# Kernel tuning notes

Measured on AMD Instinct MI355X. Metric: run time of the kernel, lower is better.

The kernel has to match this reference:

```python
import jax, jax.numpy as jnp
import numpy as np

TEMPERATURE = 0.07
EPS = 1e-8  # torch cosine_similarity clamps the norm product at eps


def setup_inputs() -> dict:
    key = jax.random.key(0)
    k1, k2 = jax.random.split(key)
    B, D = 8192, 256
    u = jax.random.normal(k1, (B, D), dtype=jnp.float32)
    v = jax.random.normal(k2, (B, D), dtype=jnp.float32)
    return {"u": u, "v": v}


def _cos_sim_matrix(a, b):
    # pairwise cosine similarity: (a . b) / max(|a||b|, eps)
    dots = a @ b.T                                   # [B, B]
    an = jnp.linalg.norm(a, axis=-1)                 # [B]
    bn = jnp.linalg.norm(b, axis=-1)                 # [B]
    denom = jnp.maximum(an[:, None] * bn[None, :], EPS)
    return dots / denom


def reference(u, v):
    B = u.shape[0]
    sim_uv = _cos_sim_matrix(u, v) / TEMPERATURE     # [B, B]
    sim_uu = _cos_sim_matrix(u, u) / TEMPERATURE     # [B, B]
    eye = jnp.eye(B, dtype=bool)
    pos_loss = jnp.diagonal(sim_uv)                  # [B]
    neg_inf = jnp.array(-jnp.inf, dtype=sim_uv.dtype)
    # off-diagonal entries of both matrices, concatenated per row (2B-2 valid each)
    negative_sim = jnp.concatenate(
        [jnp.where(eye, neg_inf, sim_uv), jnp.where(eye, neg_inf, sim_uu)], axis=1
    )                                                # [B, 2B]
    neg_loss = jax.nn.logsumexp(negative_sim, axis=-1)  # [B]
    return (-pos_loss + neg_loss).mean()
```

## Files before the change

kernel.cpp:

```cpp
#include <hip/hip_runtime.h>
#include <hip/hip_bf16.h>
#include <stdint.h>

#define NB 8192
#define ND 256
#define NW 16384
#define BM 128
#define BN 128
#define NSTRIP 4
#define STRIPW 4096
#define NTILES (STRIPW / BN)
#define NBLK 256
#define SQRT_L2E_INVT 4.5398164f
#define LN2F 0.69314718056f

typedef float floatx4 __attribute__((ext_vector_type(4)));
typedef int   intx4   __attribute__((ext_vector_type(4)));
typedef int   intx8   __attribute__((ext_vector_type(8)));

__device__ __forceinline__ void gload_lds16(const void* g, void* l) {
    __builtin_amdgcn_global_load_lds(
        (const __attribute__((address_space(1))) unsigned int*)g,
        (__attribute__((address_space(3))) unsigned int*)l,
        16, 0, 0);
}

__global__ __launch_bounds__(512) void prep_kernel(
    const float* __restrict__ u, const float* __restrict__ v,
    unsigned char* __restrict__ W, int* __restrict__ cnt)
{
    if (blockIdx.x == 0 && threadIdx.x == 0) *cnt = 0;
    const int t    = threadIdx.x;
    const int row  = blockIdx.x * 8 + (t >> 6);
    const int lane = t & 63;
    const float* src = (row < NB) ? (v + (size_t)row * ND)
                                  : (u + (size_t)(row - NB) * ND);
    float4 x = ((const float4*)src)[lane];
    float ss = x.x * x.x + x.y * x.y + x.z * x.z + x.w * x.w;
#pragma unroll
    for (int off = 1; off < 64; off <<= 1) ss += __shfl_xor(ss, off, 64);
    const float sc = rsqrtf(ss) * SQRT_L2E_INVT;
    int p = __builtin_amdgcn_cvt_pk_fp8_f32(x.x * sc, x.y * sc, 0, false);
    p     = __builtin_amdgcn_cvt_pk_fp8_f32(x.z * sc, x.w * sc, p, true);
    ((int*)(W + (size_t)row * ND))[lane] = p;
}

__global__ __launch_bounds__(512, 2) void dcl_main(
    const unsigned char* __restrict__ W,
    float* __restrict__ partial,
    float* __restrict__ pos,
    int* __restrict__ cnt,
    float* __restrict__ out)
{
    const int b  = blockIdx.x;
    const int s  = (b >> 1) & 3;
    const int rt = ((b >> 3) << 1) | (b & 1);
    const int rb = rt * BM;

    const unsigned char* A = W + (size_t)NB * ND;

    __shared__ __align__(16) char lds[98304];

    const int tid  = threadIdx.x;
    const int wave = tid >> 6;
    const int lane = tid & 63;
    const int wm   = wave >> 2;
    const int wn   = wave & 3;
    const int quad = lane >> 4;
    const int tcol = lane & 15;

    {
        const int cb0 = s * STRIPW;
#pragma unroll
        for (int i = 0; i < 4; i++) {
            int o = i * 8192 + wave * 1024 + lane * 16;
            int r = o >> 8;
            int c = (o >> 4) & 15;
            int cg = (c ^ (r & 15)) * 16;
            gload_lds16(A + (size_t)(rb + r) * ND + cg,
                        lds + i * 8192 + wave * 1024);
            gload_lds16(W + (size_t)(cb0 + r) * ND + cg,
                        lds + 32768 + i * 8192 + wave * 1024);
        }
    }
    __syncthreads();

    intx8 af[4][2];
#pragma unroll
    for (int mt = 0; mt < 4; mt++) {
        int r = wm * 64 + mt * 16 + tcol;
#pragma unroll
        for (int ks = 0; ks < 2; ks++) {
            int c0 = ks * 8 + quad * 2;
            intx4 lo = *(const intx4*)(lds + r * 256 + ((c0 ^ (r & 15)) << 4));
            intx4 hi = *(const intx4*)(lds + r * 256 + (((c0 + 1) ^ (r & 15)) << 4));
            intx8 f;
            f[0] = lo[0]; f[1] = lo[1]; f[2] = lo[2]; f[3] = lo[3];
            f[4] = hi[0]; f[5] = hi[1]; f[6] = hi[2]; f[7] = hi[3];
            af[mt][ks] = f;
        }
    }

    float rsum[4][4];
#pragma unroll
    for (int mt = 0; mt < 4; mt++)
#pragma unroll
        for (int reg = 0; reg < 4; reg++) rsum[mt][reg] = 0.f;

    for (int ct = 0; ct < NTILES; ct++) {
        char* curB = lds + 32768 + (ct & 1) * 32768;
        if (ct + 1 < NTILES) {
            char* nxt = lds + 32768 + ((ct + 1) & 1) * 32768;
            const int cbn = s * STRIPW + (ct + 1) * BN;
#pragma unroll
            for (int i = 0; i < 4; i++) {
                int o = i * 8192 + wave * 1024 + lane * 16;
                int r = o >> 8;
                int c = (o >> 4) & 15;
                int cg = (c ^ (r & 15)) * 16;
                gload_lds16(W + (size_t)(cbn + r) * ND + cg,
                            nxt + i * 8192 + wave * 1024);
            }
        }
        const int cb = s * STRIPW + ct * BN;

        intx8 bfr[2][2];
#pragma unroll
        for (int nt = 0; nt < 2; nt++) {
            int r = wn * 32 + nt * 16 + tcol;
#pragma unroll
            for (int ks = 0; ks < 2; ks++) {
                int c0 = ks * 8 + quad * 2;
                intx4 lo = *(const intx4*)(curB + r * 256 + ((c0 ^ (r & 15)) << 4));
                intx4 hi = *(const intx4*)(curB + r * 256 + (((c0 + 1) ^ (r & 15)) << 4));
                intx8 f;
                f[0] = lo[0]; f[1] = lo[1]; f[2] = lo[2]; f[3] = lo[3];
                f[4] = hi[0]; f[5] = hi[1]; f[6] = hi[2]; f[7] = hi[3];
                bfr[nt][ks] = f;
            }
        }

        floatx4 acc[4][2];
#pragma unroll
        for (int mt = 0; mt < 4; mt++)
#pragma unroll
            for (int nt = 0; nt < 2; nt++) acc[mt][nt] = (floatx4){0.f, 0.f, 0.f, 0.f};

#pragma unroll
        for (int ks = 0; ks < 2; ks++)
#pragma unroll
            for (int mt = 0; mt < 4; mt++)
#pragma unroll
                for (int nt = 0; nt < 2; nt++)
                    acc[mt][nt] = __builtin_amdgcn_mfma_scale_f32_16x16x128_f8f6f4(
                        af[mt][ks], bfr[nt][ks], acc[mt][nt],
                        0, 0,
                        0, 127,
                        0, 127);

        if (cb != rb && cb != rb + NB) {
#pragma unroll
            for (int mt = 0; mt < 4; mt++)
#pragma unroll
                for (int nt = 0; nt < 2; nt++)
#pragma unroll
                    for (int reg = 0; reg < 4; reg++)
                        rsum[mt][reg] += __builtin_amdgcn_exp2f(acc[mt][nt][reg]);
        } else {
            const bool isuv = (cb == rb);
#pragma unroll
            for (int mt = 0; mt < 4; mt++)
#pragma unroll
                for (int nt = 0; nt < 2; nt++) {
                    const int gcol = cb + wn * 32 + nt * 16 + tcol;
#pragma unroll
                    for (int reg = 0; reg < 4; reg++) {
                        const int grow = rb + wm * 64 + mt * 16 + quad * 4 + reg;
                        float sc = acc[mt][nt][reg];
                        bool diag = (gcol == grow + (isuv ? 0 : NB));
                        if (isuv && diag) pos[grow] = sc;
                        rsum[mt][reg] += diag ? 0.f : __builtin_amdgcn_exp2f(sc);
                    }
                }
        }
        __syncthreads();
    }

#pragma unroll
    for (int mt = 0; mt < 4; mt++)
#pragma unroll
        for (int reg = 0; reg < 4; reg++) {
            float vsum = rsum[mt][reg];
            vsum += __shfl_xor(vsum, 1, 64);
            vsum += __shfl_xor(vsum, 2, 64);
            vsum += __shfl_xor(vsum, 4, 64);
            vsum += __shfl_xor(vsum, 8, 64);
            if (tcol == 0) {
                int lrow = wm * 64 + mt * 16 + quad * 4 + reg;
                ((float*)lds)[wn * 128 + lrow] = vsum;
            }
        }
    __syncthreads();
    if (tid < BM) {
        const float* lf = (const float*)lds;
        partial[(size_t)s * NB + rb + tid] =
            lf[tid] + lf[128 + tid] + lf[256 + tid] + lf[384 + tid];
    }

    __threadfence();
    __syncthreads();
    __shared__ int amlast;
    if (tid == 0) amlast = (atomicAdd(cnt, 1) == NBLK - 1);
    __syncthreads();
    if (!amlast) return;
    __threadfence();

    float sacc = 0.f;
    for (int i = tid; i < NB; i += 512) {
        float tot = partial[i] + partial[NB + i] + partial[2 * NB + i]
                  + partial[3 * NB + i];
        sacc += logf(tot) - pos[i] * LN2F;
    }
#pragma unroll
    for (int off = 1; off < 64; off <<= 1) sacc += __shfl_xor(sacc, off, 64);
    __syncthreads();
    if (lane == 0) ((float*)lds)[wave] = sacc;
    __syncthreads();
    if (tid == 0) {
        const float* lf = (const float*)lds;
        float tot = 0.f;
#pragma unroll
        for (int i = 0; i < 8; i++) tot += lf[i];
        out[0] = tot / (float)NB;
    }
}

extern "C" void kernel_launch(void* const* d_in, const int* in_sizes, int n_in,
                              void* d_out, int out_size, void* d_ws, size_t ws_size,
                              hipStream_t stream) {
    const float* u = (const float*)d_in[0];
    const float* v = (const float*)d_in[1];
    float* out = (float*)d_out;

    char* ws = (char*)d_ws;
    unsigned char* W = (unsigned char*)ws;
    float* partial = (float*)(ws + (size_t)NW * ND);
    float* pos     = partial + NSTRIP * NB;
    int*   cnt     = (int*)(pos + NB);

    prep_kernel<<<NW / 8, 512, 0, stream>>>(u, v, W, cnt);
    dcl_main<<<NBLK, 512, 0, stream>>>(W, partial, pos, cnt, out);
}
```

Measured before the change: 138.7 us.

## Drop LDS staging, load B fragments directly from global with register double-buffering

Removes shared memory staging and the per-tile block barriers. Each wave now owns a 64-row by 1024-column region and loads its MFMA operand fragments straight from global/L2 into registers, double-buffered across two tiles. Per-row partial sums are combined with global atomicAdd into a zeroed rowsum array instead of a strip-partial buffer. The kernel launches 512 blocks of 256 threads. This trades LDS reuse across waves for more global/L2 traffic and atomics, in exchange for no barriers and higher block count.

Measured after the change: 167.1 us. 1.21x slower.

```diff
diff --git a/kernel.cpp b/kernel.cpp
--- a/kernel.cpp
+++ b/kernel.cpp
@@ -1,35 +1,24 @@
 #include <hip/hip_runtime.h>
-#include <hip/hip_bf16.h>
 #include <stdint.h>
 
 #define NB 8192
 #define ND 256
 #define NW 16384
-#define BM 128
-#define BN 128
-#define NSTRIP 4
-#define STRIPW 4096
-#define NTILES (STRIPW / BN)
-#define NBLK 256
+#define NBLK 512
+#define NTILE 32
 #define SQRT_L2E_INVT 4.5398164f
 #define LN2F 0.69314718056f
 
 typedef float floatx4 __attribute__((ext_vector_type(4)));
-typedef int   intx4   __attribute__((ext_vector_type(4)));
 typedef int   intx8   __attribute__((ext_vector_type(8)));
-
-__device__ __forceinline__ void gload_lds16(const void* g, void* l) {
-    __builtin_amdgcn_global_load_lds(
-        (const __attribute__((address_space(1))) unsigned int*)g,
-        (__attribute__((address_space(3))) unsigned int*)l,
-        16, 0, 0);
-}
 
 __global__ __launch_bounds__(512) void prep_kernel(
     const float* __restrict__ u, const float* __restrict__ v,
-    unsigned char* __restrict__ W, int* __restrict__ cnt)
+    unsigned char* __restrict__ W, float* __restrict__ rowsum,
+    int* __restrict__ cnt)
 {
     if (blockIdx.x == 0 && threadIdx.x == 0) *cnt = 0;
+    if (blockIdx.x < 16) rowsum[blockIdx.x * 512 + threadIdx.x] = 0.f;
     const int t    = threadIdx.x;
     const int row  = blockIdx.x * 8 + (t >> 6);
     const int lane = t & 63;
@@ -45,60 +34,91 @@
     ((int*)(W + (size_t)row * ND))[lane] = p;
 }
 
-__global__ __launch_bounds__(512, 2) void dcl_main(
+__device__ __forceinline__ void load_btile(const unsigned char* __restrict__ W,
+                                           int cb, int tcol, int quad,
+                                           intx8 (&dst)[2][2]) {
+#pragma unroll
+    for (int nt = 0; nt < 2; nt++) {
+        const unsigned char* bp = W + (size_t)(cb + nt * 16 + tcol) * ND + quad * 32;
+#pragma unroll
+        for (int ks = 0; ks < 2; ks++)
+            dst[nt][ks] = *(const intx8*)(bp + ks * 128);
+    }
+}
+
+__device__ __forceinline__ void tile_step(const intx8 (&af)[4][2],
+        const intx8 (&bt)[2][2], int cb, int rw0, float (&rsum)[4][4],
+        float* __restrict__ pos, int quad, int tcol) {
+    floatx4 acc[4][2];
+#pragma unroll
+    for (int mt = 0; mt < 4; mt++)
+#pragma unroll
+        for (int nt = 0; nt < 2; nt++) acc[mt][nt] = (floatx4){0.f, 0.f, 0.f, 0.f};
+#pragma unroll
+    for (int ks = 0; ks < 2; ks++)
+#pragma unroll
+        for (int mt = 0; mt < 4; mt++)
+#pragma unroll
+            for (int nt = 0; nt < 2; nt++)
+                acc[mt][nt] = __builtin_amdgcn_mfma_scale_f32_16x16x128_f8f6f4(
+                    af[mt][ks], bt[nt][ks], acc[mt][nt],
+                    0, 0,
+                    0, 127,
+                    0, 127);
+
+    const bool uvt = (cb >= rw0 && cb < rw0 + 64);
+    const bool uut = (cb >= rw0 + NB && cb < rw0 + NB + 64);
+    if (!uvt && !uut) {
+#pragma unroll
+        for (int mt = 0; mt < 4; mt++)
+#pragma unroll
+            for (int nt = 0; nt < 2; nt++)
+#pragma unroll
+                for (int reg = 0; reg < 4; reg++)
+                    rsum[mt][reg] += __builtin_amdgcn_exp2f(acc[mt][nt][reg]);
+    } else {
+#pragma unroll
+        for (int mt = 0; mt < 4; mt++)
+#pragma unroll
+            for (int nt = 0; nt < 2; nt++) {
+                const int gcol = cb + nt * 16 + tcol;
+#pragma unroll
+                for (int reg = 0; reg < 4; reg++) {
+                    const int grow = rw0 + mt * 16 + quad * 4 + reg;
+                    float sc = acc[mt][nt][reg];
+                    bool diag = (gcol == (uvt ? grow : grow + NB));
+                    if (uvt && diag) pos[grow] = sc;
+                    rsum[mt][reg] += diag ? 0.f : __builtin_amdgcn_exp2f(sc);
+                }
+            }
+    }
+}
+
+__global__ __launch_bounds__(256, 2) void dcl_main(
     const unsigned char* __restrict__ W,
-    float* __restrict__ partial,
+    float* __restrict__ rowsum,
     float* __restrict__ pos,
     int* __restrict__ cnt,
     float* __restrict__ out)
 {
-    const int b  = blockIdx.x;
-    const int s  = (b >> 1) & 3;
-    const int rt = ((b >> 3) << 1) | (b & 1);
-    const int rb = rt * BM;
-
-    const unsigned char* A = W + (size_t)NB * ND;
-
-    __shared__ __align__(16) char lds[98304];
-
+    const int b    = blockIdx.x;
     const int tid  = threadIdx.x;
     const int wave = tid >> 6;
     const int lane = tid & 63;
-    const int wm   = wave >> 2;
-    const int wn   = wave & 3;
     const int quad = lane >> 4;
     const int tcol = lane & 15;
+    const int rw0 = (((b >> 3) << 1) | (wave >> 1)) * 64;
+    const int cw0 = (((b & 7) << 1) | (wave & 1)) * 1024;
 
-    {
-        const int cb0 = s * STRIPW;
-#pragma unroll
-        for (int i = 0; i < 4; i++) {
-            int o = i * 8192 + wave * 1024 + lane * 16;
-            int r = o >> 8;
-            int c = (o >> 4) & 15;
-            int cg = (c ^ (r & 15)) * 16;
-            gload_lds16(A + (size_t)(rb + r) * ND + cg,
-                        lds + i * 8192 + wave * 1024);
-            gload_lds16(W + (size_t)(cb0 + r) * ND + cg,
-                        lds + 32768 + i * 8192 + wave * 1024);
-        }
-    }
-    __syncthreads();
+    const unsigned char* Au = W + (size_t)NB * ND;
 
     intx8 af[4][2];
 #pragma unroll
     for (int mt = 0; mt < 4; mt++) {
-        int r = wm * 64 + mt * 16 + tcol;
+        const unsigned char* ap = Au + (size_t)(rw0 + mt * 16 + tcol) * ND + quad * 32;
 #pragma unroll
-        for (int ks = 0; ks < 2; ks++) {
-            int c0 = ks * 8 + quad * 2;
-            intx4 lo = *(const intx4*)(lds + r * 256 + ((c0 ^ (r & 15)) << 4));
-            intx4 hi = *(const intx4*)(lds + r * 256 + (((c0 + 1) ^ (r & 15)) << 4));
-            intx8 f;
-            f[0] = lo[0]; f[1] = lo[1]; f[2] = lo[2]; f[3] = lo[3];
-            f[4] = hi[0]; f[5] = hi[1]; f[6] = hi[2]; f[7] = hi[3];
-            af[mt][ks] = f;
-        }
+        for (int ks = 0; ks < 2; ks++)
+            af[mt][ks] = *(const intx8*)(ap + ks * 128);
     }
 
     float rsum[4][4];
@@ -107,83 +127,14 @@
 #pragma unroll
         for (int reg = 0; reg < 4; reg++) rsum[mt][reg] = 0.f;
 
-    for (int ct = 0; ct < NTILES; ct++) {
-        char* curB = lds + 32768 + (ct & 1) * 32768;
-        if (ct + 1 < NTILES) {
-            char* nxt = lds + 32768 + ((ct + 1) & 1) * 32768;
-            const int cbn = s * STRIPW + (ct + 1) * BN;
-#pragma unroll
-            for (int i = 0; i < 4; i++) {
-                int o = i * 8192 + wave * 1024 + lane * 16;
-                int r = o >> 8;
-                int c = (o >> 4) & 15;
-                int cg = (c ^ (r & 15)) * 16;
-                gload_lds16(W + (size_t)(cbn + r) * ND + cg,
-                            nxt + i * 8192 + wave * 1024);
-            }
-        }
-        const int cb = s * STRIPW + ct * BN;
-
-        intx8 bfr[2][2];
-#pragma unroll
-        for (int nt = 0; nt < 2; nt++) {
-            int r = wn * 32 + nt * 16 + tcol;
-#pragma unroll
-            for (int ks = 0; ks < 2; ks++) {
-                int c0 = ks * 8 + quad * 2;
-                intx4 lo = *(const intx4*)(curB + r * 256 + ((c0 ^ (r & 15)) << 4));
-                intx4 hi = *(const intx4*)(curB + r * 256 + (((c0 + 1) ^ (r & 15)) << 4));
-                intx8 f;
-                f[0] = lo[0]; f[1] = lo[1]; f[2] = lo[2]; f[3] = lo[3];
-                f[4] = hi[0]; f[5] = hi[1]; f[6] = hi[2]; f[7] = hi[3];
-                bfr[nt][ks] = f;
-            }
-        }
-
-        floatx4 acc[4][2];
-#pragma unroll
-        for (int mt = 0; mt < 4; mt++)
-#pragma unroll
-            for (int nt = 0; nt < 2; nt++) acc[mt][nt] = (floatx4){0.f, 0.f, 0.f, 0.f};
-
-#pragma unroll
-        for (int ks = 0; ks < 2; ks++)
-#pragma unroll
-            for (int mt = 0; mt < 4; mt++)
-#pragma unroll
-                for (int nt = 0; nt < 2; nt++)
-                    acc[mt][nt] = __builtin_amdgcn_mfma_scale_f32_16x16x128_f8f6f4(
-                        af[mt][ks], bfr[nt][ks], acc[mt][nt],
-                        0, 0,
-                        0, 127,
-                        0, 127);
-
-        if (cb != rb && cb != rb + NB) {
-#pragma unroll
-            for (int mt = 0; mt < 4; mt++)
-#pragma unroll
-                for (int nt = 0; nt < 2; nt++)
-#pragma unroll
-                    for (int reg = 0; reg < 4; reg++)
-                        rsum[mt][reg] += __builtin_amdgcn_exp2f(acc[mt][nt][reg]);
-        } else {
-            const bool isuv = (cb == rb);
-#pragma unroll
-            for (int mt = 0; mt < 4; mt++)
-#pragma unroll
-                for (int nt = 0; nt < 2; nt++) {
-                    const int gcol = cb + wn * 32 + nt * 16 + tcol;
-#pragma unroll
-                    for (int reg = 0; reg < 4; reg++) {
-                        const int grow = rb + wm * 64 + mt * 16 + quad * 4 + reg;
-                        float sc = acc[mt][nt][reg];
-                        bool diag = (gcol == grow + (isuv ? 0 : NB));
-                        if (isuv && diag) pos[grow] = sc;
-                        rsum[mt][reg] += diag ? 0.f : __builtin_amdgcn_exp2f(sc);
-                    }
-                }
-        }
-        __syncthreads();
+    intx8 b0[2][2], b1[2][2];
+    load_btile(W, cw0, tcol, quad, b0);
+    for (int ct = 0; ct < NTILE; ct += 2) {
+        const int cb = cw0 + ct * 32;
+        load_btile(W, cb + 32, tcol, quad, b1);
+        tile_step(af, b0, cb, rw0, rsum, pos, quad, tcol);
+        if (ct + 2 < NTILE) load_btile(W, cb + 64, tcol, quad, b0);
+        tile_step(af, b1, cb + 32, rw0, rsum, pos, quad, tcol);
     }
 
 #pragma unroll
@@ -195,17 +146,9 @@
             vsum += __shfl_xor(vsum, 2, 64);
             vsum += __shfl_xor(vsum, 4, 64);
             vsum += __shfl_xor(vsum, 8, 64);
-            if (tcol == 0) {
-                int lrow = wm * 64 + mt * 16 + quad * 4 + reg;
-                ((float*)lds)[wn * 128 + lrow] = vsum;
-            }
+            if (tcol == 0)
+                atomicAdd(&rowsum[rw0 + mt * 16 + quad * 4 + reg], vsum);
         }
-    __syncthreads();
-    if (tid < BM) {
-        const float* lf = (const float*)lds;
-        partial[(size_t)s * NB + rb + tid] =
-            lf[tid] + lf[128 + tid] + lf[256 + tid] + lf[384 + tid];
-    }
 
     __threadfence();
     __syncthreads();
@@ -216,23 +159,15 @@
     __threadfence();
 
     float sacc = 0.f;
-    for (int i = tid; i < NB; i += 512) {
-        float tot = partial[i] + partial[NB + i] + partial[2 * NB + i]
-                  + partial[3 * NB + i];
-        sacc += logf(tot) - pos[i] * LN2F;
-    }
+    for (int i = tid; i < NB; i += 256)
+        sacc += logf(rowsum[i]) - pos[i] * LN2F;
 #pragma unroll
     for (int off = 1; off < 64; off <<= 1) sacc += __shfl_xor(sacc, off, 64);
+    __shared__ float wsum[4];
+    if (lane == 0) wsum[wave] = sacc;
     __syncthreads();
-    if (lane == 0) ((float*)lds)[wave] = sacc;
-    __syncthreads();
-    if (tid == 0) {
-        const float* lf = (const float*)lds;
-        float tot = 0.f;
-#pragma unroll
-        for (int i = 0; i < 8; i++) tot += lf[i];
-        out[0] = tot / (float)NB;
-    }
+    if (tid == 0)
+        out[0] = (wsum[0] + wsum[1] + wsum[2] + wsum[3]) / (float)NB;
 }
 
 extern "C" void kernel_launch(void* const* d_in, const int* in_sizes, int n_in,
@@ -244,10 +179,10 @@
 
     char* ws = (char*)d_ws;
     unsigned char* W = (unsigned char*)ws;
-    float* partial = (float*)(ws + (size_t)NW * ND);
-    float* pos     = partial + NSTRIP * NB;
-    int*   cnt     = (int*)(pos + NB);
+    float* rowsum = (float*)(ws + (size_t)NW * ND);
+    float* pos    = rowsum + NB;
+    int*   cnt    = (int*)(pos + NB);
 
-    prep_kernel<<<NW / 8, 512, 0, stream>>>(u, v, W, cnt);
-    dcl_main<<<NBLK, 512, 0, stream>>>(W, partial, pos, cnt, out);
+    prep_kernel<<<NW / 8, 512, 0, stream>>>(u, v, W, rowsum, cnt);
+    dcl_main<<<NBLK, 256, 0, stream>>>(W, rowsum, pos, cnt, out);
 }
```
